# Performance work log

Measured on AMD Instinct MI355X. Metric: run time of the kernel, lower is better.

Reference implementation:

```python
import jax, jax.numpy as jnp
import numpy as np

B, N, E = 8, 10000, 160000
F_IN, HID, EMB = 5, 128, 256
A_LAST, S_STEP = 10, 1


def _gcn_layer(x, src, dst, W, b, num_nodes):
    # PyG GCNConv: h = x @ W^T, add self-loops, symmetric norm, scatter-add, + bias
    h = x @ W.T
    loops = jnp.arange(num_nodes, dtype=src.dtype)
    src2 = jnp.concatenate([src, loops])
    dst2 = jnp.concatenate([dst, loops])
    deg = jax.ops.segment_sum(jnp.ones_like(dst2, dtype=h.dtype), dst2, num_segments=num_nodes)
    dinv = jnp.where(deg > 0, jax.lax.rsqrt(deg), 0.0)
    norm = dinv[src2] * dinv[dst2]                     # [E+N]
    msgs = h[src2] * norm[:, None]                     # gather + scale
    out = jax.ops.segment_sum(msgs, dst2, num_segments=num_nodes)
    return out + b


def setup_inputs() -> dict:
    key = jax.random.key(0)
    ks = jax.random.split(key, 14)
    graph_x = jax.random.normal(ks[0], (B, N, F_IN), dtype=jnp.float32)
    graph_edges = jax.random.randint(ks[1], (B, 2, E), 0, N, dtype=jnp.int64)
    position_seq = jax.random.randint(ks[2], (B,), 0, N, dtype=jnp.int64)
    available_moves = jax.random.randint(ks[3], (B, 4), 0, N, dtype=jnp.int64)
    actions = jax.random.normal(ks[4], (B, A_LAST), dtype=jnp.float32)
    steps = jax.random.normal(ks[5], (B, S_STEP), dtype=jnp.float32)

    def glorot(k, shape):
        fan_in = shape[-1]
        return jax.random.normal(k, shape, dtype=jnp.float32) / jnp.sqrt(jnp.float32(fan_in))

    proj_in = HID * 5 + A_LAST + S_STEP
    params = {
        'W1': glorot(ks[6], (HID, F_IN)), 'b1': jnp.zeros((HID,), jnp.float32),
        'W2': glorot(ks[7], (HID, HID)), 'b2': jnp.zeros((HID,), jnp.float32),
        'Wp1': glorot(ks[8], (EMB, proj_in)), 'bp1': jnp.zeros((EMB,), jnp.float32),
        'Wp2': glorot(ks[9], (EMB, EMB)), 'bp2': jnp.zeros((EMB,), jnp.float32),
    }
    return dict(graph_x=graph_x, graph_edges=graph_edges, position_seq=position_seq,
                available_moves=available_moves, actions=actions, steps=steps, **params)


def reference(graph_x, graph_edges, position_seq, available_moves, actions, steps,
              W1, b1, W2, b2, Wp1, bp1, Wp2, bp2):
    b, n, f = graph_x.shape
    num_nodes = b * n
    x = graph_x.reshape(num_nodes, f)
    addition = (jnp.arange(b, dtype=graph_edges.dtype) * n)
    ei = graph_edges + addition[:, None, None]          # [B,2,E]
    ei = jnp.swapaxes(ei, 0, 1).reshape(2, -1)          # [2, B*E]
    src, dst = ei[0], ei[1]
    position = position_seq + addition
    all_positions = jnp.concatenate(
        [available_moves + addition[:, None], position[:, None]], axis=1)  # [B,5]

    x = jax.nn.relu(_gcn_layer(x, src, dst, W1, b1, num_nodes))
    x = jax.nn.relu(_gcn_layer(x, src, dst, W2, b2, num_nodes))

    current_x = x[all_positions].reshape(b, -1)          # [B, 5*HID]
    current_x = jnp.concatenate([current_x, actions, steps], axis=-1)
    h = jax.nn.relu(current_x @ Wp1.T + bp1)
    return h @ Wp2.T + bp2
```

## Files before the change

### kernel.cpp

```cpp
#include <hip/hip_runtime.h>

#define NB 8
#define NN 10000
#define NE 160000
#define NNODES (NB*NN)
#define NEDGE (NB*NE)
#define FIN 5
#define HID 128
#define EMB 256
#define ALAST 10
#define PROJ_IN (HID*5 + ALAST + 1)
#define NPOS 40
#define E0CAP 256
#define TCAP (NPOS + NPOS*E0CAP)
#define E1C 128

#define C_NT 0
#define C_E0(t) (8 + (t)*16)

__global__ void k_mark(const int* __restrict__ avail, const int* __restrict__ pos,
                       int* __restrict__ markT, int* __restrict__ Tnodes,
                       int* __restrict__ cnts,
                       int* __restrict__ pos2t0, int* __restrict__ posNode) {
    int p = threadIdx.x;
    int n = 0;
    if (p < NPOS) {
        int b = p / 5, pi = p - b*5;
        int node = (pi < 4) ? avail[b*4 + pi] : pos[b];
        n = node + b*NN;
    }
    int firstIdx = p;
    for (int q = 0; q < NPOS; ++q) {
        int nq = __shfl(n, q, 64);
        if (p < NPOS && q < p && nq == n && firstIdx == p) firstIdx = q;
    }
    bool isFirst = (p < NPOS) && (firstIdx == p);
    unsigned long long bal = __ballot(isFirst);
    if (p < NPOS) {
        int slot = __popcll(bal & ((1ull << firstIdx) - 1ull));
        if (isFirst) {
            markT[n] = slot; Tnodes[slot] = n;
        }
        pos2t0[p] = slot; posNode[p] = n;
    }
    if (p == 0) cnts[C_NT] = __popcll(bal);
}

__global__ __launch_bounds__(256) void k_pass1(const int* __restrict__ edges,
        const int* __restrict__ markT, int* __restrict__ cnts,
        int* __restrict__ e0) {
    int idx = blockIdx.x*256 + threadIdx.x;
    int g = idx / (NE/4), w4 = idx - g*(NE/4);
    const int* base = edges + (size_t)g*2*NE;
    int4 d4 = ((const int4*)(base + NE))[w4];
    int gofs = g*NN;
    int dd[4] = {d4.x, d4.y, d4.z, d4.w};
    #pragma unroll
    for (int c = 0; c < 4; ++c) {
        int t0 = markT[gofs + dd[c]];
        if (t0 >= 0) {
            int s = base[4*w4 + c] + gofs;
            int k = atomicAdd(&cnts[C_E0(t0)], 1);
            if (k < E0CAP) e0[t0*E0CAP + k] = s;
        }
    }
}

__global__ __launch_bounds__(256) void k_dedup(const int* __restrict__ e0,
                        int* __restrict__ cnts, int* __restrict__ markT,
                        int* __restrict__ Tnodes) {
    __shared__ int lc, base;
    int t0 = blockIdx.x;
    if (threadIdx.x == 0) lc = 0;
    __syncthreads();
    int m = cnts[C_E0(t0)]; if (m > E0CAP) m = E0CAP;
    int s = -1, myIdx = -1;
    if ((int)threadIdx.x < m) {
        s = e0[t0*E0CAP + threadIdx.x];
        if (atomicCAS(&markT[s], -1, -2) == -1)
            myIdx = atomicAdd(&lc, 1);
    }
    __syncthreads();
    if (threadIdx.x == 0 && lc > 0) base = atomicAdd(&cnts[C_NT], lc);
    __syncthreads();
    if (myIdx >= 0) {
        int slot = base + myIdx;
        Tnodes[slot] = s;
        markT[s] = slot;
    }
}

__global__ __launch_bounds__(256) void k_pass2(const int* __restrict__ edges,
        int* __restrict__ markT, int* __restrict__ e1cnt, int* __restrict__ e1) {
    int idx = blockIdx.x*256 + threadIdx.x;
    int g = idx / (NE/4), w4 = idx - g*(NE/4);
    const int* base = edges + (size_t)g*2*NE;
    int4 d4 = ((const int4*)(base + NE))[w4];
    int gofs = g*NN;
    int dd[4] = {d4.x, d4.y, d4.z, d4.w};
    #pragma unroll
    for (int c = 0; c < 4; ++c) {
        int ts = markT[gofs + dd[c]];
        if (ts >= 0) {
            int s = base[4*w4 + c] + gofs;
            int k = atomicAdd(&e1cnt[ts*4], 1);
            if (k < E1C) e1[(size_t)ts*E1C + k] = s;
            if (markT[s] == -1) markT[s] = -3;
        }
    }
}

__global__ __launch_bounds__(256) void k_pass3(const int* __restrict__ edges,
        const int* __restrict__ markT, int* __restrict__ degCnt) {
    int idx = blockIdx.x*256 + threadIdx.x;
    int g = idx / (NE/4), w4 = idx - g*(NE/4);
    int4 d4 = ((const int4*)(edges + (size_t)g*2*NE + NE))[w4];
    int gofs = g*NN;
    int dd[4] = {d4.x, d4.y, d4.z, d4.w};
    #pragma unroll
    for (int c = 0; c < 4; ++c) {
        int n = gofs + dd[c];
        if (markT[n] != -1) atomicAdd(&degCnt[n], 1);
    }
}

#define KC 32
__global__ __launch_bounds__(256) void k_h12T(
        const int* __restrict__ e1cnt, const int* __restrict__ e1,
        const int* __restrict__ Tnodes,
        const int* __restrict__ degCnt, const int* __restrict__ cnts,
        const float* __restrict__ xg,
        const float* __restrict__ W1, const float* __restrict__ b1,
        const float* __restrict__ W2, float* __restrict__ hsT) {
    __shared__ float axs[FIN][128];
    __shared__ float w1s[FIN][128];
    __shared__ float b1s[128];
    __shared__ float dvs[128];
    __shared__ float xs[KC*128];
    __shared__ float wt[KC*64];
    int ntv = cnts[C_NT]; if (ntv > TCAP) ntv = TCAP;
    int jb  = blockIdx.x & 1;
    int m0g = (blockIdx.x >> 1) * 128;
    if (m0g >= ntv) return;
    int tid = threadIdx.x;
    if (tid < 128) {
        b1s[tid] = b1[tid];
        #pragma unroll
        for (int f = 0; f < FIN; ++f) w1s[f][tid] = W1[tid*FIN + f];
    } else {
        int r2 = tid - 128;
        int row = m0g + r2;
        int ok = row < ntv;
        int node = ok ? Tnodes[row] : 0;
        float dvv = ok ? rsqrtf(1.0f + (float)degCnt[node]) : 0.0f;
        dvs[r2] = dvv;
        float acc[FIN];
        #pragma unroll
        for (int f = 0; f < FIN; ++f) acc[f] = xg[(size_t)node*FIN + f]*dvv;
        if (ok) {
            int m = e1cnt[row*4]; if (m > E1C) m = E1C;
            const int* lp = e1 + (size_t)row*E1C;
            for (int j = 0; j < m; ++j) {
                int s = lp[j];
                float dv = rsqrtf(1.0f + (float)degCnt[s]);
                const float* xr = xg + (size_t)s*FIN;
                #pragma unroll
                for (int f = 0; f < FIN; ++f) acc[f] += xr[f]*dv;
            }
        }
        #pragma unroll
        for (int f = 0; f < FIN; ++f) axs[f][r2] = acc[f];
    }
    int tx = tid & 15, ty = tid >> 4;
    int m0 = ty*8;
    int j0 = tx*4;
    int r  = tid >> 1;
    int kq = (tid & 1) * 16;
    int rw  = tid >> 2;
    int kqw = (tid & 3) * 8;
    float a[8][4];
    #pragma unroll
    for (int i = 0; i < 8; ++i)
        #pragma unroll
        for (int j = 0; j < 4; ++j) a[i][j] = 0.f;
    __syncthreads();
    float axr[FIN];
    float dvr = dvs[r];
    #pragma unroll
    for (int f = 0; f < FIN; ++f) axr[f] = axs[f][r] * dvr;

    for (int kh = 0; kh < 128; kh += KC) {
        float4 wv0 = *(const float4*)&W2[(size_t)(jb*64 + rw)*128 + kh + kqw];
        float4 wv1 = *(const float4*)&W2[(size_t)(jb*64 + rw)*128 + kh + kqw + 4];
        float hv[16];
        #pragma unroll
        for (int kk = 0; kk < 16; ++kk) {
            int k1 = kh + kq + kk;
            float sv = b1s[k1];
            #pragma unroll
            for (int f = 0; f < FIN; ++f) sv += axr[f]*w1s[f][k1];
            hv[kk] = fmaxf(sv, 0.0f);
        }
        __syncthreads();
        #pragma unroll
        for (int kk = 0; kk < 16; ++kk) xs[(kq+kk)*128 + r] = hv[kk];
        wt[(kqw+0)*64 + rw] = wv0.x;
        wt[(kqw+1)*64 + rw] = wv0.y;
        wt[(kqw+2)*64 + rw] = wv0.z;
        wt[(kqw+3)*64 + rw] = wv0.w;
        wt[(kqw+4)*64 + rw] = wv1.x;
        wt[(kqw+5)*64 + rw] = wv1.y;
        wt[(kqw+6)*64 + rw] = wv1.z;
        wt[(kqw+7)*64 + rw] = wv1.w;
        __syncthreads();
        for (int k = 0; k < KC; ++k) {
            float4 xa = *(const float4*)&xs[k*128 + m0];
            float4 xb = *(const float4*)&xs[k*128 + m0 + 4];
            float4 wa = *(const float4*)&wt[k*64 + j0];
            float xr[8] = {xa.x,xa.y,xa.z,xa.w,xb.x,xb.y,xb.z,xb.w};
            #pragma unroll
            for (int i = 0; i < 8; ++i) {
                a[i][0] += xr[i]*wa.x;
                a[i][1] += xr[i]*wa.y;
                a[i][2] += xr[i]*wa.z;
                a[i][3] += xr[i]*wa.w;
            }
        }
    }
    #pragma unroll
    for (int i = 0; i < 8; ++i) {
        int row = m0g + m0 + i;
        if (row < ntv) {
            float dv = dvs[m0 + i];
            float4 v0 = make_float4(a[i][0]*dv, a[i][1]*dv, a[i][2]*dv, a[i][3]*dv);
            *(float4*)&hsT[(size_t)row*HID + jb*64 + j0] = v0;
        }
    }
}

__global__ __launch_bounds__(128) void k_aggPT(
        const int* __restrict__ pos2t0, const int* __restrict__ posNode,
        const int* __restrict__ e1cnt, const int* __restrict__ e1,
        const int* __restrict__ markT, const float* __restrict__ hsT,
        const int* __restrict__ degCnt, const float* __restrict__ b2,
        float* __restrict__ cx40) {
    int p = blockIdx.x;
    int f = threadIdx.x;
    int n = posNode[p];
    int t0 = pos2t0[p];
    float acc = hsT[(size_t)t0*HID + f];
    int m = e1cnt[t0*4]; if (m > E1C) m = E1C;
    for (int j = 0; j < m; ++j) {
        int s = e1[(size_t)t0*E1C + j];
        int ts = markT[s];
        if (ts >= 0) acc += hsT[(size_t)ts*HID + f];
    }
    float dv = rsqrtf(1.0f + (float)degCnt[n]);
    cx40[(size_t)p*HID + f] = fmaxf(acc*dv + b2[f], 0.0f);
}

__global__ __launch_bounds__(256) void k_mlp1(
        const float* __restrict__ cx40, const float* __restrict__ actions,
        const float* __restrict__ steps,
        const float* __restrict__ Wp1, const float* __restrict__ bp1,
        float* __restrict__ hm) {
    int b  = blockIdx.x >> 4;
    int jg = blockIdx.x & 15;
    int t  = threadIdx.x;
    __shared__ float c[PROJ_IN];
    for (int i = t; i < 5*HID; i += 256)
        c[i] = cx40[(size_t)b*5*HID + i];
    if (t < ALAST) c[5*HID + t] = actions[b*ALAST + t];
    if (t == ALAST) c[5*HID + ALAST] = steps[b];
    __syncthreads();
    int o = t >> 4, sub = t & 15;
    int j = jg*16 + o;
    const float* wr = Wp1 + (size_t)j*PROJ_IN;
    float s = 0.f;
    for (int k = sub; k < PROJ_IN; k += 16) s += c[k]*wr[k];
    #pragma unroll
    for (int d = 8; d; d >>= 1) s += __shfl_down(s, d, 16);
    if (sub == 0) hm[b*EMB + j] = fmaxf(s + bp1[j], 0.f);
}

__global__ __launch_bounds__(256) void k_mlp2(
        const float* __restrict__ hm, const float* __restrict__ Wp2,
        const float* __restrict__ bp2, float* __restrict__ out) {
    int b  = blockIdx.x >> 4;
    int jg = blockIdx.x & 15;
    int t  = threadIdx.x;
    __shared__ float c[EMB];
    if (t < EMB) c[t] = hm[b*EMB + t];
    __syncthreads();
    int o = t >> 4, sub = t & 15;
    int j = jg*16 + o;
    const float* wr = Wp2 + (size_t)j*EMB;
    float s = 0.f;
    for (int k = sub; k < EMB; k += 16) s += c[k]*wr[k];
    #pragma unroll
    for (int d = 8; d; d >>= 1) s += __shfl_down(s, d, 16);
    if (sub == 0) out[b*EMB + j] = s + bp2[j];
}

extern "C" void kernel_launch(void* const* d_in, const int* in_sizes, int n_in,
                              void* d_out, int out_size, void* d_ws, size_t ws_size,
                              hipStream_t stream) {
    const float* graph_x = (const float*)d_in[0];
    const int*   edges   = (const int*)d_in[1];
    const int*   pos     = (const int*)d_in[2];
    const int*   avail   = (const int*)d_in[3];
    const float* actions = (const float*)d_in[4];
    const float* steps   = (const float*)d_in[5];
    const float* W1  = (const float*)d_in[6];
    const float* b1  = (const float*)d_in[7];
    const float* W2  = (const float*)d_in[8];
    const float* b2  = (const float*)d_in[9];
    const float* Wp1 = (const float*)d_in[10];
    const float* bp1 = (const float*)d_in[11];
    const float* Wp2 = (const float*)d_in[12];
    const float* bp2 = (const float*)d_in[13];
    float* out = (float*)d_out;

    char* ws = (char*)d_ws;
    size_t off = 0;
    #define ALLOC(ptrname, type, nelem) \
        type* ptrname = (type*)(ws + off); off = (off + (size_t)(nelem)*sizeof(type) + 255) & ~(size_t)255;
    ALLOC(markT,   int,   NNODES)
    ALLOC(degCnt,  int,   NNODES)
    ALLOC(cnts,    int,   1024)
    ALLOC(e1cnt,   int,   TCAP*4)
    char* msB_end = ws + off;
    ALLOC(Tnodes,  int,   TCAP)
    ALLOC(pos2t0,  int,   NPOS)
    ALLOC(posNode, int,   NPOS)
    ALLOC(e0,      int,   NPOS*E0CAP)
    ALLOC(e1,      int,   (size_t)TCAP*E1C)
    ALLOC(hsT,     float, (size_t)TCAP*HID)
    ALLOC(cx40,    float, (size_t)NPOS*HID)
    ALLOC(hm,      float, (size_t)NB*EMB)
    #undef ALLOC

    hipMemsetAsync(markT, 0xFF, (size_t)NNODES*4, stream);
    hipMemsetAsync(degCnt, 0x00, (size_t)(msB_end - (char*)degCnt), stream);

    k_mark<<<1, 64, 0, stream>>>(avail, pos, markT, Tnodes, cnts, pos2t0, posNode);
    k_pass1<<<NEDGE/4/256, 256, 0, stream>>>(edges, markT, cnts, e0);
    k_dedup<<<NPOS, 256, 0, stream>>>(e0, cnts, markT, Tnodes);
    k_pass2<<<NEDGE/4/256, 256, 0, stream>>>(edges, markT, e1cnt, e1);
    k_pass3<<<NEDGE/4/256, 256, 0, stream>>>(edges, markT, degCnt);
    k_h12T<<<2*((TCAP+127)/128), 256, 0, stream>>>(e1cnt, e1, Tnodes, degCnt, cnts,
                                                   graph_x, W1, b1, W2, hsT);
    k_aggPT<<<NPOS, 128, 0, stream>>>(pos2t0, posNode, e1cnt, e1, markT, hsT,
                                      degCnt, b2, cx40);
    k_mlp1<<<NB*16, 256, 0, stream>>>(cx40, actions, steps, Wp1, bp1, hm);
    k_mlp2<<<NB*16, 256, 0, stream>>>(hm, Wp2, bp2, out);
}
```

Before: 177.5 us.

## Fuse memsets into clear kernel, fold T-node degrees into pass2, merge aggregation into MLP1

Replaces two hipMemsetAsync calls with a single clear kernel. Degree counting for T nodes now happens inside pass2, which already visits their incoming edges, so pass3 only counts neighbour nodes marked -3. The final position aggregation kernel is folded into mlp1, so each MLP block recomputes the five position embeddings it needs instead of reading cx40. This removes launches and an intermediate buffer, but repeats the aggregation 16 times per batch element.

```diff
diff --git a/kernel.cpp b/kernel.cpp
--- a/kernel.cpp
+++ b/kernel.cpp
@@ -14,9 +14,18 @@
 #define E0CAP 256
 #define TCAP (NPOS + NPOS*E0CAP)
 #define E1C 128
+#define NBLK ((NNODES+255)/256)
 
 #define C_NT 0
 #define C_E0(t) (8 + (t)*16)
+
+__global__ void k_clear(int* __restrict__ markT, int* __restrict__ degCnt,
+                        int* __restrict__ cnts, int* __restrict__ e1cnt) {
+    int i = blockIdx.x*256 + threadIdx.x;
+    if (i < NNODES) { markT[i] = -1; degCnt[i] = 0; }
+    if (i < 1024) cnts[i] = 0;
+    for (int j = i; j < TCAP*4; j += NNODES) e1cnt[j] = 0;
+}
 
 __global__ void k_mark(const int* __restrict__ avail, const int* __restrict__ pos,
                        int* __restrict__ markT, int* __restrict__ Tnodes,
@@ -91,7 +100,8 @@
 }
 
 __global__ __launch_bounds__(256) void k_pass2(const int* __restrict__ edges,
-        int* __restrict__ markT, int* __restrict__ e1cnt, int* __restrict__ e1) {
+        int* __restrict__ markT, int* __restrict__ e1cnt, int* __restrict__ e1,
+        int* __restrict__ degCnt) {
     int idx = blockIdx.x*256 + threadIdx.x;
     int g = idx / (NE/4), w4 = idx - g*(NE/4);
     const int* base = edges + (size_t)g*2*NE;
@@ -100,11 +110,13 @@
     int dd[4] = {d4.x, d4.y, d4.z, d4.w};
     #pragma unroll
     for (int c = 0; c < 4; ++c) {
-        int ts = markT[gofs + dd[c]];
+        int d = gofs + dd[c];
+        int ts = markT[d];
         if (ts >= 0) {
             int s = base[4*w4 + c] + gofs;
             int k = atomicAdd(&e1cnt[ts*4], 1);
             if (k < E1C) e1[(size_t)ts*E1C + k] = s;
+            atomicAdd(&degCnt[d], 1);
             if (markT[s] == -1) markT[s] = -3;
         }
     }
@@ -120,7 +132,7 @@
     #pragma unroll
     for (int c = 0; c < 4; ++c) {
         int n = gofs + dd[c];
-        if (markT[n] != -1) atomicAdd(&degCnt[n], 1);
+        if (markT[n] == -3) atomicAdd(&degCnt[n], 1);
     }
 }
 
@@ -238,38 +250,45 @@
     }
 }
 
-__global__ __launch_bounds__(128) void k_aggPT(
+__global__ __launch_bounds__(256) void k_mlp1(
         const int* __restrict__ pos2t0, const int* __restrict__ posNode,
         const int* __restrict__ e1cnt, const int* __restrict__ e1,
         const int* __restrict__ markT, const float* __restrict__ hsT,
         const int* __restrict__ degCnt, const float* __restrict__ b2,
-        float* __restrict__ cx40) {
-    int p = blockIdx.x;
-    int f = threadIdx.x;
-    int n = posNode[p];
-    int t0 = pos2t0[p];
-    float acc = hsT[(size_t)t0*HID + f];
-    int m = e1cnt[t0*4]; if (m > E1C) m = E1C;
-    for (int j = 0; j < m; ++j) {
-        int s = e1[(size_t)t0*E1C + j];
-        int ts = markT[s];
-        if (ts >= 0) acc += hsT[(size_t)ts*HID + f];
-    }
-    float dv = rsqrtf(1.0f + (float)degCnt[n]);
-    cx40[(size_t)p*HID + f] = fmaxf(acc*dv + b2[f], 0.0f);
-}
-
-__global__ __launch_bounds__(256) void k_mlp1(
-        const float* __restrict__ cx40, const float* __restrict__ actions,
-        const float* __restrict__ steps,
+        const float* __restrict__ actions, const float* __restrict__ steps,
         const float* __restrict__ Wp1, const float* __restrict__ bp1,
         float* __restrict__ hm) {
     int b  = blockIdx.x >> 4;
     int jg = blockIdx.x & 15;
     int t  = threadIdx.x;
     __shared__ float c[PROJ_IN];
-    for (int i = t; i < 5*HID; i += 256)
-        c[i] = cx40[(size_t)b*5*HID + i];
+    __shared__ int slots[5*E1C];
+    __shared__ int cm[5], t0s[5];
+    __shared__ float dvP[5];
+    if (t < 5) {
+        int t0 = pos2t0[b*5 + t];
+        t0s[t] = t0;
+        int m = e1cnt[t0*4]; if (m > E1C) m = E1C;
+        cm[t] = m;
+        dvP[t] = rsqrtf(1.0f + (float)degCnt[posNode[b*5 + t]]);
+    }
+    __syncthreads();
+    for (int i = t; i < 5*E1C; i += 256) {
+        int p5 = i >> 7, j = i & (E1C-1);
+        if (j < cm[p5]) slots[i] = markT[e1[(size_t)t0s[p5]*E1C + j]];
+    }
+    __syncthreads();
+    for (int i = t; i < 5*HID; i += 256) {
+        int p5 = i >> 7, f = i & 127;
+        float acc = hsT[(size_t)t0s[p5]*HID + f];
+        int m = cm[p5];
+        const int* sp = &slots[p5*E1C];
+        for (int j = 0; j < m; ++j) {
+            int ts = sp[j];
+            if (ts >= 0) acc += hsT[(size_t)ts*HID + f];
+        }
+        c[i] = fmaxf(acc*dvP[p5] + b2[f], 0.0f);
+    }
     if (t < ALAST) c[5*HID + t] = actions[b*ALAST + t];
     if (t == ALAST) c[5*HID + ALAST] = steps[b];
     __syncthreads();
@@ -329,29 +348,24 @@
     ALLOC(degCnt,  int,   NNODES)
     ALLOC(cnts,    int,   1024)
     ALLOC(e1cnt,   int,   TCAP*4)
-    char* msB_end = ws + off;
     ALLOC(Tnodes,  int,   TCAP)
     ALLOC(pos2t0,  int,   NPOS)
     ALLOC(posNode, int,   NPOS)
     ALLOC(e0,      int,   NPOS*E0CAP)
     ALLOC(e1,      int,   (size_t)TCAP*E1C)
     ALLOC(hsT,     float, (size_t)TCAP*HID)
-    ALLOC(cx40,    float, (size_t)NPOS*HID)
     ALLOC(hm,      float, (size_t)NB*EMB)
     #undef ALLOC
 
-    hipMemsetAsync(markT, 0xFF, (size_t)NNODES*4, stream);
-    hipMemsetAsync(degCnt, 0x00, (size_t)(msB_end - (char*)degCnt), stream);
-
+    k_clear<<<NBLK, 256, 0, stream>>>(markT, degCnt, cnts, e1cnt);
     k_mark<<<1, 64, 0, stream>>>(avail, pos, markT, Tnodes, cnts, pos2t0, posNode);
     k_pass1<<<NEDGE/4/256, 256, 0, stream>>>(edges, markT, cnts, e0);
     k_dedup<<<NPOS, 256, 0, stream>>>(e0, cnts, markT, Tnodes);
-    k_pass2<<<NEDGE/4/256, 256, 0, stream>>>(edges, markT, e1cnt, e1);
+    k_pass2<<<NEDGE/4/256, 256, 0, stream>>>(edges, markT, e1cnt, e1, degCnt);
     k_pass3<<<NEDGE/4/256, 256, 0, stream>>>(edges, markT, degCnt);
     k_h12T<<<2*((TCAP+127)/128), 256, 0, stream>>>(e1cnt, e1, Tnodes, degCnt, cnts,
                                                    graph_x, W1, b1, W2, hsT);
-    k_aggPT<<<NPOS, 128, 0, stream>>>(pos2t0, posNode, e1cnt, e1, markT, hsT,
-                                      degCnt, b2, cx40);
-    k_mlp1<<<NB*16, 256, 0, stream>>>(cx40, actions, steps, Wp1, bp1, hm);
+    k_mlp1<<<NB*16, 256, 0, stream>>>(pos2t0, posNode, e1cnt, e1, markT, hsT,
+                                      degCnt, b2, actions, steps, Wp1, bp1, hm);
     k_mlp2<<<NB*16, 256, 0, stream>>>(hm, Wp2, bp2, out);
 }
```

Measured after the change: 177.7 us. Within noise of the previous version (+0.1%).
